# Kernel tuning notes

Hardware: AMD Instinct MI355X
Metric: run time of the kernel (lower is better)

Reference implementation:

```python
import jax, jax.numpy as jnp
import numpy as np

M, N, F = 512, 128, 512  # molecules, atoms per molecule, feature dim
HID, OUT = F // 4, 1


def setup_inputs() -> dict:
    key = jax.random.key(0)
    k1, k2, k3 = jax.random.split(key, 3)
    h = jax.random.normal(k1, (M, N, F), dtype=jnp.float32)
    W1 = jax.random.normal(k2, (F, HID), dtype=jnp.float32) * (1.0 / np.sqrt(F))
    b1 = jnp.zeros((HID,), dtype=jnp.float32)
    W2 = jax.random.normal(k3, (HID, OUT), dtype=jnp.float32) * (1.0 / np.sqrt(HID))
    b2 = jnp.zeros((OUT,), dtype=jnp.float32)
    return {"h": h, "W1": W1, "b1": b1, "W2": W2, "b2": b2}


def reference(h, W1, b1, W2, b2):
    # method == 'weighted_summation'
    # gate MLP: Linear -> ReLU -> Linear -> Sigmoid, per atom
    w = jax.nn.sigmoid(jax.nn.relu(h @ W1 + b1) @ W2 + b2)  # [M, N, OUT]
    # per-molecule weighted sum over atoms: mm(w_h.T, h) for each molecule,
    # concatenated along dim 0 -> [M*OUT, F] (OUT=1 -> [M, F])
    out = jnp.einsum('mno,mnf->mof', w, h)  # [M, OUT, F]
    return out.reshape(M * OUT, F)
```

## Files before the change

### kernel.cpp

```cpp
#include <hip/hip_runtime.h>
#include <hip/hip_bf16.h>


typedef unsigned short u16;
typedef unsigned int u32;
typedef __bf16 bf16x8 __attribute__((ext_vector_type(8)));
typedef float f32x4 __attribute__((ext_vector_type(4)));
typedef float f32x2 __attribute__((ext_vector_type(2)));
typedef u32 u32x4 __attribute__((ext_vector_type(4)));

#define M_MOL 512
#define N_ATOM 128
#define F_DIM 512
#define HID_DIM 128

static __device__ __forceinline__ u16 f2bf(float x) {
  u32 u = __float_as_uint(x);
  u32 r = (u + 0x7fffu + ((u >> 16) & 1u)) >> 16;
  return (u16)r;
}
static __device__ __forceinline__ bf16x8 pack8(u32x4 a, u32x4 b) {
  u32x4 r;
  r[0] = (a[0] >> 16) | (a[1] & 0xffff0000u);
  r[1] = (a[2] >> 16) | (a[3] & 0xffff0000u);
  r[2] = (b[0] >> 16) | (b[1] & 0xffff0000u);
  r[3] = (b[2] >> 16) | (b[3] & 0xffff0000u);
  return __builtin_bit_cast(bf16x8, r);
}

__global__ __launch_bounds__(256) void transpose_w1(const float* __restrict__ W1,
                                                    u16* __restrict__ W1Tt) {
  __shared__ float tile[64][65];
  const int k0 = blockIdx.x * 64;
  const int n0 = blockIdx.y * 64;
  const int t = threadIdx.x;
  #pragma unroll
  for (int i = 0; i < 16; ++i) {
    const int lin = i * 256 + t;
    const int lr = lin >> 6, lc = lin & 63;
    tile[lc][lr] = W1[(size_t)(k0 + lr) * HID_DIM + (n0 + lc)];
  }
  __syncthreads();
  #pragma unroll
  for (int i = 0; i < 16; ++i) {
    const int lin = i * 256 + t;
    const int wr = lin >> 6, wc = lin & 63;
    const int k = k0 + wc;
    W1Tt[(size_t)(k >> 5) * (HID_DIM * 32) + (size_t)(n0 + wr) * 32 + (k & 31)] =
        f2bf(tile[wr][wc]);
  }
}

__global__ __launch_bounds__(256) void gate_pass(
    const float* __restrict__ h, const u16* __restrict__ W1Tt,
    const float* __restrict__ b1, const float* __restrict__ W2,
    const float* __restrict__ b2, float* __restrict__ wbuf) {
  const int tid = threadIdx.x;
  const int wv = tid >> 6;
  const int lane = tid & 63;
  const int quad = lane >> 4;
  const int cl = lane & 15;

  const int row0 = blockIdx.x * 64 + wv * 16;
  const u32x4* ap = (const u32x4*)(h + (size_t)(row0 + cl) * F_DIM) + quad * 2;
  const u16* bg = W1Tt + cl * 32 + quad * 8;

  f32x4 acc[8];
  #pragma unroll
  for (int t = 0; t < 8; ++t) acc[t] = (f32x4){0.f, 0.f, 0.f, 0.f};

  u32x4 aC0 = ap[0], aC1 = ap[1];
  u32x4 bC[8];
  #pragma unroll
  for (int t = 0; t < 8; ++t) bC[t] = *(const u32x4*)(bg + t * 512);

  #pragma unroll
  for (int ks = 0; ks < 16; ++ks) {
    u32x4 aN0, aN1, bN[8];
    if (ks < 15) {
      aN0 = ap[(ks + 1) * 8];
      aN1 = ap[(ks + 1) * 8 + 1];
      #pragma unroll
      for (int t = 0; t < 8; ++t)
        bN[t] = *(const u32x4*)(bg + (size_t)(ks + 1) * (HID_DIM * 32) + t * 512);
    }
    bf16x8 afr = pack8(aC0, aC1);
    #pragma unroll
    for (int t = 0; t < 8; ++t)
      acc[t] = __builtin_amdgcn_mfma_f32_16x16x32_bf16(
          afr, __builtin_bit_cast(bf16x8, bC[t]), acc[t], 0, 0, 0);
    aC0 = aN0; aC1 = aN1;
    #pragma unroll
    for (int t = 0; t < 8; ++t) bC[t] = bN[t];
  }

  float psum[4] = {0.f, 0.f, 0.f, 0.f};
  #pragma unroll
  for (int t = 0; t < 8; ++t) {
    const int hid = t * 16 + cl;
    const float b1v = b1[hid];
    const float w2v = W2[hid];
    #pragma unroll
    for (int r = 0; r < 4; ++r) {
      float tv = fmaxf(acc[t][r] + b1v, 0.f);
      psum[r] = fmaf(tv, w2v, psum[r]);
    }
  }
  #pragma unroll
  for (int off = 1; off < 16; off <<= 1)
    #pragma unroll
    for (int r = 0; r < 4; ++r)
      psum[r] += __shfl_xor(psum[r], off, 64);
  if (cl == 0) {
    const float b2v = b2[0];
    #pragma unroll
    for (int r = 0; r < 4; ++r)
      wbuf[row0 + quad * 4 + r] = 1.f / (1.f + __expf(-(psum[r] + b2v)));
  }
}

__global__ __launch_bounds__(256) void weight_pass(
    const float* __restrict__ h, const float* __restrict__ wbuf,
    float* __restrict__ out) {
  const int m = blockIdx.x;
  const int f0 = threadIdx.x * 2;
  const float* hm = h + (size_t)m * (N_ATOM * F_DIM);
  const float* wm = wbuf + (size_t)m * N_ATOM;

  float a0 = 0.f, a1 = 0.f;
  #pragma unroll 2
  for (int n0 = 0; n0 < N_ATOM; n0 += 8) {
    f32x2 v[8];
    #pragma unroll
    for (int j = 0; j < 8; ++j)
      v[j] = *(const f32x2*)(hm + (size_t)(n0 + j) * F_DIM + f0);
    #pragma unroll
    for (int j = 0; j < 8; ++j) {
      const float wn = wm[n0 + j];
      a0 = fmaf(wn, v[j][0], a0);
      a1 = fmaf(wn, v[j][1], a1);
    }
  }
  f32x2 o; o[0] = a0; o[1] = a1;
  *(f32x2*)(out + (size_t)m * F_DIM + f0) = o;
}

extern "C" void kernel_launch(void* const* d_in, const int* in_sizes, int n_in,
                              void* d_out, int out_size, void* d_ws, size_t ws_size,
                              hipStream_t stream) {
  const float* h  = (const float*)d_in[0];
  const float* W1 = (const float*)d_in[1];
  const float* b1 = (const float*)d_in[2];
  const float* W2 = (const float*)d_in[3];
  const float* b2 = (const float*)d_in[4];
  float* out = (float*)d_out;

  u16* W1Tt = (u16*)d_ws;
  float* wbuf = (float*)((char*)d_ws + (size_t)HID_DIM * F_DIM * sizeof(u16));

  transpose_w1<<<dim3(8, 2), 256, 0, stream>>>(W1, W1Tt);
  gate_pass<<<M_MOL * 2, 256, 0, stream>>>(h, W1Tt, b1, W2, b2, wbuf);
  weight_pass<<<M_MOL, 256, 0, stream>>>(h, wbuf, out);
}
```

Baseline: 227.5 us.

## Fuse gate MLP and weighted pooling into one per-molecule kernel

Replaces the separate gate and weighted-sum kernels with one kernel per molecule. Each block stages the transposed bf16 W1 in shared memory and keeps its atom rows in registers as bf16. It computes the sigmoid gate weights into shared memory, then reuses those register-resident bf16 rows for the weighted sum using cross-lane shuffles and a shared-memory reduction. The aim is to read h from global memory once instead of twice and to drop the intermediate weight buffer. In exchange the pooled output is now computed from truncated bf16 values rather than fp32 h, and the large shared-memory footprint limits occupancy.

```diff
diff --git a/kernel.cpp b/kernel.cpp
--- a/kernel.cpp
+++ b/kernel.cpp
@@ -6,7 +6,6 @@
 typedef unsigned int u32;
 typedef __bf16 bf16x8 __attribute__((ext_vector_type(8)));
 typedef float f32x4 __attribute__((ext_vector_type(4)));
-typedef float f32x2 __attribute__((ext_vector_type(2)));
 typedef u32 u32x4 __attribute__((ext_vector_type(4)));
 
 #define M_MOL 512
@@ -51,47 +50,58 @@
   }
 }
 
-__global__ __launch_bounds__(256) void gate_pass(
+__global__ __launch_bounds__(512, 2) void pool_mol(
     const float* __restrict__ h, const u16* __restrict__ W1Tt,
     const float* __restrict__ b1, const float* __restrict__ W2,
-    const float* __restrict__ b2, float* __restrict__ wbuf) {
+    const float* __restrict__ b2, float* __restrict__ out) {
+  __shared__ u16 Bs[16 * HID_DIM * 32];
+  __shared__ float red[8][F_DIM];
+  __shared__ float w_s[N_ATOM];
+
+  const int m = blockIdx.x;
   const int tid = threadIdx.x;
   const int wv = tid >> 6;
   const int lane = tid & 63;
   const int quad = lane >> 4;
   const int cl = lane & 15;
 
-  const int row0 = blockIdx.x * 64 + wv * 16;
-  const u32x4* ap = (const u32x4*)(h + (size_t)(row0 + cl) * F_DIM) + quad * 2;
-  const u16* bg = W1Tt + cl * 32 + quad * 8;
+  {
+    const u32x4* src = (const u32x4*)W1Tt;
+    u32x4* dst = (u32x4*)Bs;
+    #pragma unroll
+    for (int i = 0; i < 16; ++i)
+      dst[i * 512 + tid] = src[i * 512 + tid];
+  }
+
+  const int row = wv * 16 + cl;
+  const float* hr = h + ((size_t)m * N_ATOM + row) * F_DIM;
+  const u32x4* ap = (const u32x4*)hr + quad * 2;
+  bf16x8 ah[16];
+  {
+    u32x4 a32[32];
+    #pragma unroll
+    for (int ks = 0; ks < 16; ++ks) {
+      a32[2 * ks]     = ap[ks * 8];
+      a32[2 * ks + 1] = ap[ks * 8 + 1];
+    }
+    #pragma unroll
+    for (int ks = 0; ks < 16; ++ks)
+      ah[ks] = pack8(a32[2 * ks], a32[2 * ks + 1]);
+  }
+  __syncthreads();
 
   f32x4 acc[8];
   #pragma unroll
   for (int t = 0; t < 8; ++t) acc[t] = (f32x4){0.f, 0.f, 0.f, 0.f};
 
-  u32x4 aC0 = ap[0], aC1 = ap[1];
-  u32x4 bC[8];
-  #pragma unroll
-  for (int t = 0; t < 8; ++t) bC[t] = *(const u32x4*)(bg + t * 512);
-
   #pragma unroll
   for (int ks = 0; ks < 16; ++ks) {
-    u32x4 aN0, aN1, bN[8];
-    if (ks < 15) {
-      aN0 = ap[(ks + 1) * 8];
-      aN1 = ap[(ks + 1) * 8 + 1];
-      #pragma unroll
-      for (int t = 0; t < 8; ++t)
-        bN[t] = *(const u32x4*)(bg + (size_t)(ks + 1) * (HID_DIM * 32) + t * 512);
+    const u16* bt = Bs + ks * (HID_DIM * 32) + cl * 32 + quad * 8;
+    #pragma unroll
+    for (int t = 0; t < 8; ++t) {
+      bf16x8 bfr = *(const bf16x8*)(bt + t * 512);
+      acc[t] = __builtin_amdgcn_mfma_f32_16x16x32_bf16(ah[ks], bfr, acc[t], 0, 0, 0);
     }
-    bf16x8 afr = pack8(aC0, aC1);
-    #pragma unroll
-    for (int t = 0; t < 8; ++t)
-      acc[t] = __builtin_amdgcn_mfma_f32_16x16x32_bf16(
-          afr, __builtin_bit_cast(bf16x8, bC[t]), acc[t], 0, 0, 0);
-    aC0 = aN0; aC1 = aN1;
-    #pragma unroll
-    for (int t = 0; t < 8; ++t) bC[t] = bN[t];
   }
 
   float psum[4] = {0.f, 0.f, 0.f, 0.f};
@@ -115,34 +125,44 @@
     const float b2v = b2[0];
     #pragma unroll
     for (int r = 0; r < 4; ++r)
-      wbuf[row0 + quad * 4 + r] = 1.f / (1.f + __expf(-(psum[r] + b2v)));
+      w_s[wv * 16 + quad * 4 + r] = 1.f / (1.f + __expf(-(psum[r] + b2v)));
   }
-}
+  asm volatile("s_waitcnt lgkmcnt(0)" ::: "memory");
+  __builtin_amdgcn_sched_barrier(0);
 
-__global__ __launch_bounds__(256) void weight_pass(
-    const float* __restrict__ h, const float* __restrict__ wbuf,
-    float* __restrict__ out) {
-  const int m = blockIdx.x;
-  const int f0 = threadIdx.x * 2;
-  const float* hm = h + (size_t)m * (N_ATOM * F_DIM);
-  const float* wm = wbuf + (size_t)m * N_ATOM;
-
-  float a0 = 0.f, a1 = 0.f;
-  #pragma unroll 2
-  for (int n0 = 0; n0 < N_ATOM; n0 += 8) {
-    f32x2 v[8];
+  const float wn = w_s[wv * 16 + cl];
+  float fout[8];
+  #pragma unroll
+  for (int ks = 0; ks < 16; ++ks) {
+    u32x4 uv = __builtin_bit_cast(u32x4, ah[ks]);
+    float p[8];
     #pragma unroll
-    for (int j = 0; j < 8; ++j)
-      v[j] = *(const f32x2*)(hm + (size_t)(n0 + j) * F_DIM + f0);
+    for (int j = 0; j < 4; ++j) {
+      p[2 * j]     = wn * __uint_as_float(uv[j] << 16);
+      p[2 * j + 1] = wn * __uint_as_float(uv[j] & 0xffff0000u);
+    }
     #pragma unroll
-    for (int j = 0; j < 8; ++j) {
-      const float wn = wm[n0 + j];
-      a0 = fmaf(wn, v[j][0], a0);
-      a1 = fmaf(wn, v[j][1], a1);
+    for (int off = 1; off < 16; off <<= 1)
+      #pragma unroll
+      for (int j = 0; j < 8; ++j)
+        p[j] += __shfl_xor(p[j], off, 64);
+    if (cl == ks) {
+      #pragma unroll
+      for (int j = 0; j < 8; ++j) fout[j] = p[j];
     }
   }
-  f32x2 o; o[0] = a0; o[1] = a1;
-  *(f32x2*)(out + (size_t)m * F_DIM + f0) = o;
+
+  #pragma unroll
+  for (int j = 0; j < 8; ++j) red[wv][cl * 32 + quad * 8 + j] = fout[j];
+  __syncthreads();
+
+  {
+    const int f = tid;
+    float o = 0.f;
+    #pragma unroll
+    for (int w = 0; w < 8; ++w) o += red[w][f];
+    out[(size_t)m * F_DIM + f] = o;
+  }
 }
 
 extern "C" void kernel_launch(void* const* d_in, const int* in_sizes, int n_in,
@@ -156,9 +176,7 @@
   float* out = (float*)d_out;
 
   u16* W1Tt = (u16*)d_ws;
-  float* wbuf = (float*)((char*)d_ws + (size_t)HID_DIM * F_DIM * sizeof(u16));
 
   transpose_w1<<<dim3(8, 2), 256, 0, stream>>>(W1, W1Tt);
-  gate_pass<<<M_MOL * 2, 256, 0, stream>>>(h, W1Tt, b1, W2, b2, wbuf);
-  weight_pass<<<M_MOL, 256, 0, stream>>>(h, wbuf, out);
+  pool_mol<<<M_MOL, 512, 0, stream>>>(h, W1Tt, b1, W2, b2, out);
 }
```

Result: no change. 226.0 us (-0.6%).
